# Kernel optimization log

Hardware: AMD Instinct MI355X
Metric: run time of the kernel (lower is better)

The kernel has to match this reference:

```python
import jax, jax.numpy as jnp
import numpy as np

N = 256            # state_space_size
BF = (4, 4, 4)     # branching_factors
T = 128            # time steps
D_IN = 64          # input_size
D_T = 64           # time_embedding_size
BATCH = 16
NUM_NODES = N * 4 * 4 * 4  # 16384


def setup_inputs() -> dict:
    key = jax.random.key(0)
    ks = jax.random.split(key, 20)

    def lin_w(k, out_d, in_d):
        return jax.random.normal(k, (out_d, in_d), jnp.float32) / np.sqrt(in_d)

    inp = {
        "x": jax.random.normal(ks[0], (BATCH, T, N), jnp.float32),
        "t_embeddings_schedule": jax.random.normal(ks[1], (T, D_T), jnp.float32),
        "input_vector": jax.random.normal(ks[2], (BATCH, T, D_IN), jnp.float32),
        # Fanout node params
        "Wa": lin_w(ks[3], NUM_NODES, N),
        "ba": jnp.zeros((NUM_NODES,), jnp.float32),
        "Wt": lin_w(ks[4], NUM_NODES, D_T),
        "Wi": lin_w(ks[5], NUM_NODES, D_IN),
        # Node with bf[:3]=[4,4,4]: reduces last 4 -> [N,4,4]
        "w3": jax.random.normal(ks[6], (N, 4, 4, 4), jnp.float32) * np.sqrt(2.0 / (4 + N * 16)),
        "tW3": lin_w(ks[7], N * 16, D_T),
        "tb3": jnp.zeros((N * 16,), jnp.float32),
        # Node with bf[:2]=[4,4]
        "w2": jax.random.normal(ks[8], (N, 4, 4), jnp.float32) * np.sqrt(2.0 / (4 + N * 4)),
        "tW2": lin_w(ks[9], N * 4, D_T),
        "tb2": jnp.zeros((N * 4,), jnp.float32),
        # Node with bf[:1]=[4]
        "w1": jax.random.normal(ks[10], (N, 4), jnp.float32) * np.sqrt(2.0 / (4 + N)),
        "tW1": lin_w(ks[11], N, D_T),
        "tb1": jnp.zeros((N,), jnp.float32),
    }
    return inp


def _node(act, t_emb, w, tW, tb):
    # act: [..., T, N, *bf]; w: [N, *bf]; reduce last branching dim
    tproj = (t_emb @ tW.T + tb).reshape(t_emb.shape[0], *w.shape[:-1])  # [T, N, *bf[:-1]]
    pre = (w * act).sum(-1) + tproj  # broadcast over leading batch dims
    return jax.nn.softplus(pre)


def reference(x, t_embeddings_schedule, input_vector, Wa, ba, Wt, Wi,
              w3, tW3, tb3, w2, tW2, tb2, w1, tW1, tb1):
    t_emb = t_embeddings_schedule
    # Fanout: [B, T, N] -> [B, T, N, 4, 4, 4]
    pre = x @ Wa.T + ba + (t_emb @ Wt.T) + input_vector @ Wi.T  # [B, T, NUM_NODES]
    act = jax.nn.softplus(pre.reshape(*pre.shape[:-1], N, *BF))
    # Tree: deepest node first (insert-at-1 order in original)
    act = _node(act, t_emb, w3, tW3, tb3)  # [B, T, N, 4, 4]
    act = _node(act, t_emb, w2, tW2, tb2)  # [B, T, N, 4]
    act = _node(act, t_emb, w1, tW1, tb1)  # [B, T, N]
    return act
```

## Files before the change

### kernel.cpp

```cpp
#include <hip/hip_runtime.h>

typedef __attribute__((ext_vector_type(16))) float f32x16;
typedef __attribute__((ext_vector_type(8))) __bf16 bf16x8;
typedef __attribute__((ext_vector_type(8))) unsigned short u16x8;

__device__ __forceinline__ unsigned short f2bf(float f) {
    unsigned int u = __float_as_uint(f);
    u += 0x7fffu + ((u >> 16) & 1u);
    return (unsigned short)(u >> 16);
}

__device__ __forceinline__ float softplus_f(float x) {
    float e = __expf(-fabsf(x));
    return fmaxf(x, 0.0f) + __logf(1.0f + e);
}

#define REPACK_NB 2
#define REPACK_BLOCKS 1728
__global__ __launch_bounds__(256) void repack(
        const float* __restrict__ x, const float* __restrict__ iv,
        const float* __restrict__ temb,
        const float* __restrict__ Wa, const float* __restrict__ Wi,
        const float* __restrict__ Wt,
        unsigned short* __restrict__ Abf2 ) {
    const int stride = REPACK_BLOCKS * 256;
    const int tid0 = blockIdx.x * 256 + threadIdx.x;
    float4 f[REPACK_NB][2];
    int dsto[REPACK_NB];
    #pragma unroll
    for (int c = 0; c < REPACK_NB; ++c) {
        const int idx = tid0 + c * stride;
        const bool isA = idx < 98304;
        const int widx = isA ? idx : idx - 98304;
        const int row = widx / 48;
        const int kc  = widx % 48;
        const int kk  = kc * 8;
        const float* p0 = isA ? (x    + (size_t)row * 256) : (Wa + (size_t)row * 256);
        const float* p1 = isA ? (iv   + (size_t)row * 64)  : (Wi + (size_t)row * 64);
        const float* p2 = isA ? (temb + (size_t)(row & 127) * 64) : (Wt + (size_t)row * 64);
        const float* src = (kk < 256) ? (p0 + kk) : ((kk < 320) ? (p1 + kk - 256) : (p2 + kk - 320));
        f[c][0] = ((const float4*)src)[0];
        f[c][1] = ((const float4*)src)[1];
        const int g  = row >> 5;
        const int r31 = row & 31;
        const int kp = kc >> 1;
        const int h  = kc & 1;
        const int o  = ((g * 24 + kp) * 64) + h * 32 + r31;
        dsto[c] = (isA ? o : (98304 + o));
    }
    #pragma unroll
    for (int c = 0; c < REPACK_NB; ++c) {
        u16x8 o;
        o[0] = f2bf(f[c][0].x); o[1] = f2bf(f[c][0].y); o[2] = f2bf(f[c][0].z); o[3] = f2bf(f[c][0].w);
        o[4] = f2bf(f[c][1].x); o[5] = f2bf(f[c][1].y); o[6] = f2bf(f[c][1].z); o[7] = f2bf(f[c][1].w);
        *(u16x8*)(Abf2 + (size_t)dsto[c] * 8) = o;
    }
}

__global__ __launch_bounds__(256) void tproj(
        const float* __restrict__ temb,
        const float* __restrict__ tW3, const float* __restrict__ tb3,
        const float* __restrict__ tW2, const float* __restrict__ tb2,
        const float* __restrict__ tW1, const float* __restrict__ tb1,
        float* __restrict__ tp3T, float* __restrict__ tp2T, float* __restrict__ tp1T) {
    __shared__ float se[32 * 64];
    const int tid = threadIdx.x;
    const int tbase = blockIdx.y * 32;
    for (int i = tid; i < 32 * 64; i += 256) se[i] = temb[tbase * 64 + i];
    __syncthreads();
    const int j = blockIdx.x * 64 + (tid >> 2);
    const float* W; const float* bias; float* outp; int jl;
    if      (j < 4096) { W = tW3; bias = tb3; outp = tp3T; jl = j; }
    else if (j < 5120) { W = tW2; bias = tb2; outp = tp2T; jl = j - 4096; }
    else               { W = tW1; bias = tb1; outp = tp1T; jl = j - 5120; }
    float4 wreg[16];
    const float4* wrow = (const float4*)(W + (size_t)jl * 64);
    #pragma unroll
    for (int k = 0; k < 16; ++k) wreg[k] = wrow[k];
    const float b = bias[jl];
    #pragma unroll
    for (int s = 0; s < 8; ++s) {
        const int tl = (tid & 3) + s * 4;
        const float4* e4 = (const float4*)&se[tl * 64];
        float a = b;
        #pragma unroll
        for (int k = 0; k < 16; ++k) {
            float4 e = e4[k];
            a += wreg[k].x * e.x + wreg[k].y * e.y + wreg[k].z * e.z + wreg[k].w * e.w;
        }
        outp[(size_t)jl * 128 + tbase + tl] = a;
    }
}

__global__ __launch_bounds__(256, 3)
void fused_gemm_tree(const unsigned short* __restrict__ Wbf2,
                     const unsigned short* __restrict__ Abf2,
                     const float* __restrict__ ba,
                     const float* __restrict__ tp3T, const float* __restrict__ tp2T,
                     const float* __restrict__ tp1T,
                     const float* __restrict__ w3, const float* __restrict__ w2,
                     const float* __restrict__ w1,
                     float* __restrict__ out) {
    const int tid  = threadIdx.x;
    const int wave = tid >> 6;
    const int lane = tid & 63;
    const int wr = wave >> 1;
    const int wc = wave & 1;
    const int lane31 = lane & 31;
    const int h = lane >> 5;

    const int node0 = blockIdx.x * 128;
    const int m0    = blockIdx.y * 128;

    f32x16 acc[2][2];
    #pragma unroll
    for (int fm = 0; fm < 2; ++fm)
        #pragma unroll
        for (int cf = 0; cf < 2; ++cf)
            #pragma unroll
            for (int r = 0; r < 16; ++r) acc[fm][cf][r] = 0.0f;

    const unsigned short* aW0 = Wbf2 + (size_t)(blockIdx.x * 4 + wr * 2 + 0) * 24 * 512;
    const unsigned short* aW1 = aW0 + 24 * 512;
    const unsigned short* aA0 = Abf2 + (size_t)(blockIdx.y * 4 + wc * 2 + 0) * 24 * 512;
    const unsigned short* aA1 = aA0 + 24 * 512;
    const int lo = lane * 8;

    #pragma unroll
    for (int kp = 0; kp < 24; ++kp) {
        const int off = kp * 512 + lo;
        bf16x8 af0 = *(const bf16x8*)(aW0 + off);
        bf16x8 af1 = *(const bf16x8*)(aW1 + off);
        bf16x8 bf0 = *(const bf16x8*)(aA0 + off);
        bf16x8 bf1 = *(const bf16x8*)(aA1 + off);
        acc[0][0] = __builtin_amdgcn_mfma_f32_32x32x16_bf16(af0, bf0, acc[0][0], 0, 0, 0);
        acc[0][1] = __builtin_amdgcn_mfma_f32_32x32x16_bf16(af0, bf1, acc[0][1], 0, 0, 0);
        acc[1][0] = __builtin_amdgcn_mfma_f32_32x32x16_bf16(af1, bf0, acc[1][0], 0, 0, 0);
        acc[1][1] = __builtin_amdgcn_mfma_f32_32x32x16_bf16(af1, bf1, acc[1][1], 0, 0, 0);
    }

    const int n = blockIdx.x * 2 + wr;
    const int t0 = wc * 64 + lane31;

    float4 bav[2][4], w3v[2][4];
    #pragma unroll
    for (int fm = 0; fm < 2; ++fm)
        #pragma unroll
        for (int s2 = 0; s2 < 4; ++s2) {
            const int leafbase = fm * 32 + 8 * s2 + 4 * h;
            bav[fm][s2] = *(const float4*)&ba[node0 + wr * 64 + leafbase];
            w3v[fm][s2] = *(const float4*)&w3[n * 64 + leafbase];
        }
    float w2v[4][2], w1v[4];
    #pragma unroll
    for (int i = 0; i < 4; ++i) {
        #pragma unroll
        for (int s2b = 0; s2b < 2; ++s2b)
            w2v[i][s2b] = w2[n * 16 + i * 4 + 2 * s2b + h];
        w1v[i] = w1[n * 4 + i];
    }
    float tp3v[2][2][4], tp2v[2][2][2], tp1v[2];
    #pragma unroll
    for (int fm = 0; fm < 2; ++fm)
        #pragma unroll
        for (int cf = 0; cf < 2; ++cf) {
            const int t = t0 + cf * 32;
            #pragma unroll
            for (int s2 = 0; s2 < 4; ++s2) {
                const int i  = fm * 2 + (s2 >> 1);
                const int jj = 2 * (s2 & 1) + h;
                tp3v[fm][cf][s2] = tp3T[(size_t)((n * 4 + i) * 4 + jj) * 128 + t];
            }
            #pragma unroll
            for (int b = 0; b < 2; ++b)
                tp2v[fm][cf][b] = tp2T[(size_t)(n * 4 + fm * 2 + b) * 128 + t];
        }
    #pragma unroll
    for (int cf = 0; cf < 2; ++cf) tp1v[cf] = tp1T[(size_t)n * 128 + t0 + cf * 32];

    float s1[2] = {0.0f, 0.0f};
    #pragma unroll
    for (int fm = 0; fm < 2; ++fm) {
        #pragma unroll
        for (int cf = 0; cf < 2; ++cf) {
            #pragma unroll
            for (int b = 0; b < 2; ++b) {
                float cs = 0.0f;
                #pragma unroll
                for (int s2b = 0; s2b < 2; ++s2b) {
                    const int s2 = 2 * b + s2b;
                    float p3 = 0.0f;
                    const float* bv = (const float*)&bav[fm][s2];
                    const float* wv = (const float*)&w3v[fm][s2];
                    #pragma unroll
                    for (int l = 0; l < 4; ++l) {
                        float a0 = softplus_f(acc[fm][cf][s2 * 4 + l] + bv[l]);
                        p3 = fmaf(a0, wv[l], p3);
                    }
                    float a3 = softplus_f(p3 + tp3v[fm][cf][s2]);
                    cs = fmaf(a3, w2v[fm * 2 + b][s2b], cs);
                }
                float Q = cs + __shfl_xor(cs, 32);
                float a2 = softplus_f(Q + tp2v[fm][cf][b]);
                s1[cf] = fmaf(a2, w1v[fm * 2 + b], s1[cf]);
            }
        }
    }
    {
        const float sj = h ? s1[1] : s1[0];
        const float tq = h ? tp1v[1] : tp1v[0];
        const int t = t0 + h * 32;
        out[(size_t)(m0 + t) * 256 + n] = softplus_f(sj + tq);
    }
}

extern "C" void kernel_launch(void* const* d_in, const int* in_sizes, int n_in,
                              void* d_out, int out_size, void* d_ws, size_t ws_size,
                              hipStream_t stream) {
    const float* x    = (const float*)d_in[0];
    const float* temb = (const float*)d_in[1];
    const float* iv   = (const float*)d_in[2];
    const float* Wa   = (const float*)d_in[3];
    const float* ba   = (const float*)d_in[4];
    const float* Wt   = (const float*)d_in[5];
    const float* Wi   = (const float*)d_in[6];
    const float* w3   = (const float*)d_in[7];
    const float* tW3  = (const float*)d_in[8];
    const float* tb3  = (const float*)d_in[9];
    const float* w2   = (const float*)d_in[10];
    const float* tW2  = (const float*)d_in[11];
    const float* tb2  = (const float*)d_in[12];
    const float* w1   = (const float*)d_in[13];
    const float* tW1  = (const float*)d_in[14];
    const float* tb1  = (const float*)d_in[15];
    float* out = (float*)d_out;

    char* ws = (char*)d_ws;
    unsigned short* Abf2 = (unsigned short*)(ws);
    unsigned short* Wbf2 = (unsigned short*)(ws + 1572864);
    float* tp3T = (float*)(ws + 14155776);
    float* tp2T = (float*)(ws + 16252928);
    float* tp1T = (float*)(ws + 16777216);

    repack<<<dim3(REPACK_BLOCKS), dim3(256), 0, stream>>>(x, iv, temb, Wa, Wi, Wt, Abf2);
    tproj<<<dim3(84, 4), dim3(256), 0, stream>>>(temb, tW3, tb3, tW2, tb2, tW1, tb1,
                                                 tp3T, tp2T, tp1T);
    fused_gemm_tree<<<dim3(128, 16), dim3(256), 0, stream>>>(Wbf2, Abf2, ba, tp3T, tp2T, tp1T,
                                                             w3, w2, w1, out);
}
```

Baseline: 160.8 us.

## Stage repack through LDS and pre-swizzle time projections into lane-contiguous layout

The repack kernel now loads 32 rows per block into shared memory with coalesced float4 reads, then emits the bf16 MFMA-fragment layout with contiguous stores, replacing the scattered per-thread gather. The tproj kernel writes its outputs directly in the per-lane order the GEMM epilogue consumes, so the epilogue replaces many strided scalar loads with a few vector loads. The occupancy hint on the fused GEMM rises from 3 to 4 blocks per SM. Costs are an LDS-staging barrier in repack, duplicated tp2/tp1 writes, and possible register pressure under the tighter launch bound.

```diff
diff --git a/kernel.cpp b/kernel.cpp
--- a/kernel.cpp
+++ b/kernel.cpp
@@ -1,6 +1,8 @@
 #include <hip/hip_runtime.h>
 
 typedef __attribute__((ext_vector_type(16))) float f32x16;
+typedef __attribute__((ext_vector_type(4)))  float f32x4v;
+typedef __attribute__((ext_vector_type(2)))  float f32x2v;
 typedef __attribute__((ext_vector_type(8))) __bf16 bf16x8;
 typedef __attribute__((ext_vector_type(8))) unsigned short u16x8;
 
@@ -15,45 +17,46 @@
     return fmaxf(x, 0.0f) + __logf(1.0f + e);
 }
 
-#define REPACK_NB 2
-#define REPACK_BLOCKS 1728
-__global__ __launch_bounds__(256) void repack(
+#define RP_STRIDE 388
+__global__ __launch_bounds__(256) void repack2(
         const float* __restrict__ x, const float* __restrict__ iv,
         const float* __restrict__ temb,
         const float* __restrict__ Wa, const float* __restrict__ Wi,
         const float* __restrict__ Wt,
-        unsigned short* __restrict__ Abf2 ) {
-    const int stride = REPACK_BLOCKS * 256;
-    const int tid0 = blockIdx.x * 256 + threadIdx.x;
-    float4 f[REPACK_NB][2];
-    int dsto[REPACK_NB];
-    #pragma unroll
-    for (int c = 0; c < REPACK_NB; ++c) {
-        const int idx = tid0 + c * stride;
-        const bool isA = idx < 98304;
-        const int widx = isA ? idx : idx - 98304;
-        const int row = widx / 48;
-        const int kc  = widx % 48;
-        const int kk  = kc * 8;
+        unsigned short* __restrict__ Out ) {
+    __shared__ float se[32 * RP_STRIDE];
+    const int g = blockIdx.x;
+    const bool isA = g < 64;
+    const int gr = isA ? g : g - 64;
+    const int tid = threadIdx.x;
+    #pragma unroll
+    for (int q = 0; q < 12; ++q) {
+        const int fi = q * 256 + tid;
+        const int r  = fi / 96;
+        const int c4 = fi % 96;
+        const int k  = c4 * 4;
+        const int row = gr * 32 + r;
         const float* p0 = isA ? (x    + (size_t)row * 256) : (Wa + (size_t)row * 256);
         const float* p1 = isA ? (iv   + (size_t)row * 64)  : (Wi + (size_t)row * 64);
         const float* p2 = isA ? (temb + (size_t)(row & 127) * 64) : (Wt + (size_t)row * 64);
-        const float* src = (kk < 256) ? (p0 + kk) : ((kk < 320) ? (p1 + kk - 256) : (p2 + kk - 320));
-        f[c][0] = ((const float4*)src)[0];
-        f[c][1] = ((const float4*)src)[1];
-        const int g  = row >> 5;
-        const int r31 = row & 31;
-        const int kp = kc >> 1;
-        const int h  = kc & 1;
-        const int o  = ((g * 24 + kp) * 64) + h * 32 + r31;
-        dsto[c] = (isA ? o : (98304 + o));
-    }
-    #pragma unroll
-    for (int c = 0; c < REPACK_NB; ++c) {
+        const float* src = (k < 256) ? (p0 + k) : ((k < 320) ? (p1 + k - 256) : (p2 + k - 320));
+        *(float4*)&se[r * RP_STRIDE + k] = *(const float4*)src;
+    }
+    __syncthreads();
+    unsigned short* dst = Out + (size_t)g * 1536 * 8;
+    #pragma unroll
+    for (int q = 0; q < 6; ++q) {
+        const int chunk = q * 256 + tid;
+        const int kp   = chunk >> 6;
+        const int lane = chunk & 63;
+        const int h    = lane >> 5;
+        const int r31  = lane & 31;
+        const int k0   = (kp * 2 + h) * 8;
+        const float* s = &se[r31 * RP_STRIDE + k0];
         u16x8 o;
-        o[0] = f2bf(f[c][0].x); o[1] = f2bf(f[c][0].y); o[2] = f2bf(f[c][0].z); o[3] = f2bf(f[c][0].w);
-        o[4] = f2bf(f[c][1].x); o[5] = f2bf(f[c][1].y); o[6] = f2bf(f[c][1].z); o[7] = f2bf(f[c][1].w);
-        *(u16x8*)(Abf2 + (size_t)dsto[c] * 8) = o;
+        o[0] = f2bf(s[0]); o[1] = f2bf(s[1]); o[2] = f2bf(s[2]); o[3] = f2bf(s[3]);
+        o[4] = f2bf(s[4]); o[5] = f2bf(s[5]); o[6] = f2bf(s[6]); o[7] = f2bf(s[7]);
+        *(u16x8*)(dst + (size_t)chunk * 8) = o;
     }
 }
 
@@ -62,17 +65,17 @@
         const float* __restrict__ tW3, const float* __restrict__ tb3,
         const float* __restrict__ tW2, const float* __restrict__ tb2,
         const float* __restrict__ tW1, const float* __restrict__ tb1,
-        float* __restrict__ tp3T, float* __restrict__ tp2T, float* __restrict__ tp1T) {
+        float* __restrict__ tp3E, float* __restrict__ tp2E, float* __restrict__ tp1E) {
     __shared__ float se[32 * 64];
     const int tid = threadIdx.x;
     const int tbase = blockIdx.y * 32;
     for (int i = tid; i < 32 * 64; i += 256) se[i] = temb[tbase * 64 + i];
     __syncthreads();
     const int j = blockIdx.x * 64 + (tid >> 2);
-    const float* W; const float* bias; float* outp; int jl;
-    if      (j < 4096) { W = tW3; bias = tb3; outp = tp3T; jl = j; }
-    else if (j < 5120) { W = tW2; bias = tb2; outp = tp2T; jl = j - 4096; }
-    else               { W = tW1; bias = tb1; outp = tp1T; jl = j - 5120; }
+    const float* W; const float* bias; int jl, region;
+    if      (j < 4096) { W = tW3; bias = tb3; jl = j;        region = 0; }
+    else if (j < 5120) { W = tW2; bias = tb2; jl = j - 4096; region = 1; }
+    else               { W = tW1; bias = tb1; jl = j - 5120; region = 2; }
     float4 wreg[16];
     const float4* wrow = (const float4*)(W + (size_t)jl * 64);
     #pragma unroll
@@ -81,6 +84,7 @@
     #pragma unroll
     for (int s = 0; s < 8; ++s) {
         const int tl = (tid & 3) + s * 4;
+        const int t  = tbase + tl;
         const float4* e4 = (const float4*)&se[tl * 64];
         float a = b;
         #pragma unroll
@@ -88,16 +92,33 @@
             float4 e = e4[k];
             a += wreg[k].x * e.x + wreg[k].y * e.y + wreg[k].z * e.z + wreg[k].w * e.w;
         }
-        outp[(size_t)jl * 128 + tbase + tl] = a;
-    }
-}
-
-__global__ __launch_bounds__(256, 3)
+        const int wc = t >> 6, cf = (t >> 5) & 1, l31 = t & 31;
+        if (region == 0) {
+            const int n = jl >> 4, i = (jl >> 2) & 3, jj = jl & 3;
+            const int fm = i >> 1, s2 = ((i & 1) << 1) | (jj >> 1), h = jj & 1;
+            const int lane = (h << 5) | l31;
+            tp3E[(size_t)((((n * 2 + wc) * 2 + fm) * 2 + cf) * 64 + lane) * 4 + s2] = a;
+        } else if (region == 1) {
+            const int n = jl >> 2, i = jl & 3;
+            const int fm = i >> 1, bb = i & 1;
+            #pragma unroll
+            for (int h = 0; h < 2; ++h)
+                tp2E[(size_t)((((n * 2 + wc) * 2 + fm) * 2 + cf) * 64 + h * 32 + l31) * 2 + bb] = a;
+        } else {
+            const int n = jl;
+            #pragma unroll
+            for (int h = 0; h < 2; ++h)
+                tp1E[(size_t)((n * 2 + wc) * 64 + h * 32 + l31) * 2 + cf] = a;
+        }
+    }
+}
+
+__global__ __launch_bounds__(256, 4)
 void fused_gemm_tree(const unsigned short* __restrict__ Wbf2,
                      const unsigned short* __restrict__ Abf2,
                      const float* __restrict__ ba,
-                     const float* __restrict__ tp3T, const float* __restrict__ tp2T,
-                     const float* __restrict__ tp1T,
+                     const float* __restrict__ tp3E, const float* __restrict__ tp2E,
+                     const float* __restrict__ tp1E,
                      const float* __restrict__ w3, const float* __restrict__ w2,
                      const float* __restrict__ w1,
                      float* __restrict__ out) {
@@ -141,6 +162,7 @@
 
     const int n = blockIdx.x * 2 + wr;
     const int t0 = wc * 64 + lane31;
+    const int nbase = n * 2 + wc;
 
     float4 bav[2][4], w3v[2][4];
     #pragma unroll
@@ -159,24 +181,16 @@
             w2v[i][s2b] = w2[n * 16 + i * 4 + 2 * s2b + h];
         w1v[i] = w1[n * 4 + i];
     }
-    float tp3v[2][2][4], tp2v[2][2][2], tp1v[2];
+    f32x4v t3[2][2]; f32x2v t2[2][2]; f32x2v t1;
     #pragma unroll
     for (int fm = 0; fm < 2; ++fm)
         #pragma unroll
         for (int cf = 0; cf < 2; ++cf) {
-            const int t = t0 + cf * 32;
-            #pragma unroll
-            for (int s2 = 0; s2 < 4; ++s2) {
-                const int i  = fm * 2 + (s2 >> 1);
-                const int jj = 2 * (s2 & 1) + h;
-                tp3v[fm][cf][s2] = tp3T[(size_t)((n * 4 + i) * 4 + jj) * 128 + t];
-            }
-            #pragma unroll
-            for (int b = 0; b < 2; ++b)
-                tp2v[fm][cf][b] = tp2T[(size_t)(n * 4 + fm * 2 + b) * 128 + t];
-        }
-    #pragma unroll
-    for (int cf = 0; cf < 2; ++cf) tp1v[cf] = tp1T[(size_t)n * 128 + t0 + cf * 32];
+            const size_t base = (size_t)((nbase * 2 + fm) * 2 + cf) * 64 + lane;
+            t3[fm][cf] = ((const f32x4v*)tp3E)[base];
+            t2[fm][cf] = ((const f32x2v*)tp2E)[base];
+        }
+    t1 = ((const f32x2v*)tp1E)[(size_t)nbase * 64 + lane];
 
     float s1[2] = {0.0f, 0.0f};
     #pragma unroll
@@ -197,18 +211,18 @@
                         float a0 = softplus_f(acc[fm][cf][s2 * 4 + l] + bv[l]);
                         p3 = fmaf(a0, wv[l], p3);
                     }
-                    float a3 = softplus_f(p3 + tp3v[fm][cf][s2]);
+                    float a3 = softplus_f(p3 + t3[fm][cf][s2]);
                     cs = fmaf(a3, w2v[fm * 2 + b][s2b], cs);
                 }
                 float Q = cs + __shfl_xor(cs, 32);
-                float a2 = softplus_f(Q + tp2v[fm][cf][b]);
+                float a2 = softplus_f(Q + t2[fm][cf][b]);
                 s1[cf] = fmaf(a2, w1v[fm * 2 + b], s1[cf]);
             }
         }
     }
     {
         const float sj = h ? s1[1] : s1[0];
-        const float tq = h ? tp1v[1] : tp1v[0];
+        const float tq = h ? t1[1] : t1[0];
         const int t = t0 + h * 32;
         out[(size_t)(m0 + t) * 256 + n] = softplus_f(sj + tq);
     }
@@ -238,13 +252,13 @@
     char* ws = (char*)d_ws;
     unsigned short* Abf2 = (unsigned short*)(ws);
     unsigned short* Wbf2 = (unsigned short*)(ws + 1572864);
-    float* tp3T = (float*)(ws + 14155776);
-    float* tp2T = (float*)(ws + 16252928);
-    float* tp1T = (float*)(ws + 16777216);
-
-    repack<<<dim3(REPACK_BLOCKS), dim3(256), 0, stream>>>(x, iv, temb, Wa, Wi, Wt, Abf2);
+    float* tp3E = (float*)(ws + 14155776);
+    float* tp2E = (float*)(ws + 16252928);
+    float* tp1E = (float*)(ws + 17301504);
+
+    repack2<<<dim3(576), dim3(256), 0, stream>>>(x, iv, temb, Wa, Wi, Wt, Abf2);
     tproj<<<dim3(84, 4), dim3(256), 0, stream>>>(temb, tW3, tb3, tW2, tb2, tW1, tb1,
-                                                 tp3T, tp2T, tp1T);
-    fused_gemm_tree<<<dim3(128, 16), dim3(256), 0, stream>>>(Wbf2, Abf2, ba, tp3T, tp2T, tp1T,
+                                                 tp3E, tp2E, tp1E);
+    fused_gemm_tree<<<dim3(128, 16), dim3(256), 0, stream>>>(Wbf2, Abf2, ba, tp3E, tp2E, tp1E,
                                                              w3, w2, w1, out);
 }
```

Result: slower. 170.1 us (+5.8%).
